# Performance work log

Measured on AMD Instinct MI355X. Metric: run time of the kernel, lower is better.

## Reference

```python
import jax, jax.numpy as jnp
import numpy as np


def _dsconv(x, dw_w, dw_b, pw_w, pw_b):
    # depthwise 3x3 (padding=1, stride=1) + pointwise 1x1, both with bias (PyTorch Conv2d default)
    C = x.shape[1]
    y = jax.lax.conv_general_dilated(
        x, dw_w, window_strides=(1, 1), padding=((1, 1), (1, 1)),
        dimension_numbers=('NCHW', 'OIHW', 'NCHW'), feature_group_count=C)
    y = y + dw_b[None, :, None, None]
    y = jnp.einsum('bchw,oc->bohw', y, pw_w) + pw_b[None, :, None, None]
    return y


def setup_inputs() -> dict:
    key = jax.random.key(0)
    ks = jax.random.split(key, 16)
    B, C, H, W = 8, 256, 64, 256
    inp = {"x": jax.random.normal(ks[0], (B, C, H, W), dtype=jnp.float32)}
    chans = [(C, 128), (128, 64), (64, 32), (32, 9)]
    ki = 1
    for li, (ci, co) in enumerate(chans, start=1):
        inp[f"dw{li}_w"] = jax.random.normal(ks[ki], (ci, 1, 3, 3), dtype=jnp.float32) / 3.0; ki += 1
        inp[f"dw{li}_b"] = jnp.zeros((ci,), dtype=jnp.float32)
        inp[f"pw{li}_w"] = jax.random.normal(ks[ki], (co, ci), dtype=jnp.float32) / jnp.sqrt(jnp.float32(ci)); ki += 1
        inp[f"pw{li}_b"] = jnp.zeros((co,), dtype=jnp.float32)
    return inp


def reference(x,
              dw1_w, dw1_b, pw1_w, pw1_b,
              dw2_w, dw2_b, pw2_w, pw2_b,
              dw3_w, dw3_b, pw3_w, pw3_b,
              dw4_w, dw4_b, pw4_w, pw4_b):
    # la_conv stack: DSConv->ReLU x3, final DSConv (no relu), out channels = 9
    a = jax.nn.relu(_dsconv(x, dw1_w, dw1_b, pw1_w, pw1_b))
    a = jax.nn.relu(_dsconv(a, dw2_w, dw2_b, pw2_w, pw2_b))
    a = jax.nn.relu(_dsconv(a, dw3_w, dw3_b, pw3_w, pw3_b))
    a = _dsconv(a, dw4_w, dw4_b, pw4_w, pw4_b)            # (B,9,H,W)
    attn = jax.nn.softmax(a, axis=1)                      # softmax over the 9 taps

    B, C, H, W = x.shape
    xpad = jnp.pad(x, ((0, 0), (0, 0), (1, 1), (1, 1)))
    # dynamic 3x3 conv: out[b,c,i,j] = sum_{ki,kj} xpad[b,c,i+ki,j+kj] * attn[b,ki*3+kj,i,j]
    out = jnp.zeros_like(x)
    for ki in range(3):
        for kj in range(3):
            out = out + xpad[:, :, ki:ki + H, kj:kj + W] * attn[:, ki * 3 + kj][:, None, :, :]

    char_attn = attn.transpose(0, 2, 3, 1).reshape(B, H, W, 3, 3)
    return out, char_attn
```

## Files before the change

kernel.cpp:

```cpp
#include <hip/hip_runtime.h>
#include <math.h>

#define BH_ 64
#define BW_ 256
constexpr size_t HW = (size_t)BH_ * BW_;

using f32x4   = __attribute__((ext_vector_type(4))) float;
using short8  = __attribute__((ext_vector_type(8))) short;
using short4v = __attribute__((ext_vector_type(4))) short;

__device__ __forceinline__ short f2bf(float f) {
    unsigned u = __float_as_uint(f);
    u += 0x7fffu + ((u >> 16) & 1u);
    return (short)(u >> 16);
}
__device__ __forceinline__ float bf2f(short s) {
    return __uint_as_float(((unsigned)(unsigned short)s) << 16);
}

__device__ __forceinline__ int xcd_swizzle() {
    const int rb  = blockIdx.x;
    const int cpx = gridDim.x >> 3;
    return (rb & 7) * cpx + (rb >> 3);
}

__global__ __launch_bounds__(256)
void prep_kernel(const float* __restrict__ p1,
                 const float* __restrict__ p2,
                 const float* __restrict__ p3,
                 short* __restrict__ wb1,
                 short* __restrict__ wb2,
                 float* __restrict__ wt3)
{
    int idx = blockIdx.x * 256 + threadIdx.x;
    if (idx < 128 * 256) {
        wb1[idx] = f2bf(p1[idx]);
    } else if (idx < 128 * 256 + 64 * 128) {
        int r = idx - 128 * 256;
        wb2[r] = f2bf(p2[r]);
    } else if (idx < 128 * 256 + 64 * 128 + 32 * 64) {
        int r = idx - (128 * 256 + 64 * 128);
        int ci = r / 32, co = r % 32;
        wt3[r] = p3[co * 64 + ci];
    }
}

template<int CI, int CO, bool INBF>
__global__ __launch_bounds__(256, 4)
void dsconv_mfma(const void* __restrict__ xin_,
                 const float* __restrict__ dww,
                 const float* __restrict__ dwb,
                 const short* __restrict__ wBf,
                 const float* __restrict__ pwb,
                 short* __restrict__ out)
{
    constexpr int CIC = 32;
    constexpr int PX  = 64;
    constexpr int NT  = CO / 16;
    constexpr int WNT = NT / 4;
    constexpr int ST  = CI + 8;
    constexpr int NC  = CI / CIC;
    static_assert(NT % 4 == 0 && CI % CIC == 0, "geometry");

    __shared__ short Abuf[PX * ST];

    const int t    = threadIdx.x;
    const int w    = t >> 6;
    const int lane = t & 63;
    const int bid  = xcd_swizzle();
    const int jt   = bid & 3;
    const int i    = (bid >> 2) & 63;
    const int b    = bid >> 8;
    const int j0   = jt * PX;

    const int ci_l = t >> 3;
    const int g    = t & 7;
    const int jq   = j0 + g * 8;
    const bool vtop = (i > 0), vbot = (i < BH_ - 1);

    const int lm = lane & 15;
    const int kb = lane >> 4;

    {
        const int aswz = ((jq >> 3) & 7) << 3;
        #pragma unroll
        for (int c = 0; c < NC; ++c) {
            const int cc = c * CIC;
            const int ci = cc + ci_l;

            float xw[3][10];
            #pragma unroll
            for (int di = 0; di < 3; ++di) {
                const bool ok = (di == 0) ? vtop : (di == 2) ? vbot : true;
                if (ok) {
                    if constexpr (INBF) {
                        const short* xp = (const short*)xin_ + ((size_t)b * CI + ci) * HW;
                        const short* xr = xp + (size_t)(i + di - 1) * BW_ + jq;
                        xw[di][0] = (jq > 0) ? bf2f(xr[-1]) : 0.f;
                        short8 S = *reinterpret_cast<const short8*>(xr);
                        #pragma unroll
                        for (int e = 0; e < 8; ++e) xw[di][1 + e] = bf2f(S[e]);
                        xw[di][9] = (jq + 8 < BW_) ? bf2f(xr[8]) : 0.f;
                    } else {
                        const float* xp = (const float*)xin_ + ((size_t)b * CI + ci) * HW;
                        const float* xr = xp + (size_t)(i + di - 1) * BW_ + jq;
                        xw[di][0] = (jq > 0) ? xr[-1] : 0.f;
                        float4 A = *reinterpret_cast<const float4*>(xr);
                        float4 Bq = *reinterpret_cast<const float4*>(xr + 4);
                        xw[di][1] = A.x; xw[di][2] = A.y; xw[di][3] = A.z; xw[di][4] = A.w;
                        xw[di][5] = Bq.x; xw[di][6] = Bq.y; xw[di][7] = Bq.z; xw[di][8] = Bq.w;
                        xw[di][9] = (jq + 8 < BW_) ? xr[8] : 0.f;
                    }
                } else {
                    #pragma unroll
                    for (int e = 0; e < 10; ++e) xw[di][e] = 0.f;
                }
            }

            const float* wkp = dww + ci * 9;
            float o[8];
            {
                const float dwbv = dwb[ci];
                #pragma unroll
                for (int e = 0; e < 8; ++e) o[e] = dwbv;
            }
            #pragma unroll
            for (int di = 0; di < 3; ++di) {
                const float w0 = wkp[di * 3 + 0];
                const float w1 = wkp[di * 3 + 1];
                const float w2 = wkp[di * 3 + 2];
                #pragma unroll
                for (int e = 0; e < 8; ++e)
                    o[e] += w0 * xw[di][e] + w1 * xw[di][e + 1] + w2 * xw[di][e + 2];
            }
            #pragma unroll
            for (int e = 0; e < 8; ++e) {
                int px = g * 8 + e;
                int sa = (px * ST + ci) ^ aswz;
                Abuf[sa] = f2bf(o[e]);
            }
        }
    }

    __syncthreads();

    f32x4 acc[4][WNT];
    #pragma unroll
    for (int q = 0; q < WNT; ++q) {
        float bv = pwb[(w * WNT + q) * 16 + lm];
        #pragma unroll
        for (int mt = 0; mt < 4; ++mt) {
            f32x4 z = {bv, bv, bv, bv};
            acc[mt][q] = z;
        }
    }

    const short* bbase[WNT];
    #pragma unroll
    for (int q = 0; q < WNT; ++q)
        bbase[q] = wBf + (size_t)((w * WNT + q) * 16 + lm) * CI + kb * 8;

    short8 bcur[WNT], bnxt[WNT];
    #pragma unroll
    for (int q = 0; q < WNT; ++q)
        bcur[q] = *reinterpret_cast<const short8*>(bbase[q]);

    #pragma unroll
    for (int c = 0; c < NC; ++c) {
        if (c + 1 < NC) {
            #pragma unroll
            for (int q = 0; q < WNT; ++q)
                bnxt[q] = *reinterpret_cast<const short8*>(bbase[q] + (c + 1) * CIC);
        }
        #pragma unroll
        for (int mt = 0; mt < 4; ++mt) {
            int px = mt * 16 + lm;
            int sa = (px * ST + c * CIC + kb * 8) ^ (((px >> 3) & 7) << 3);
            short8 af = *reinterpret_cast<const short8*>(&Abuf[sa]);
            #pragma unroll
            for (int q = 0; q < WNT; ++q)
                acc[mt][q] = __builtin_amdgcn_mfma_f32_16x16x32_bf16(
                    af, bcur[q], acc[mt][q], 0, 0, 0);
        }
        #pragma unroll
        for (int q = 0; q < WNT; ++q) bcur[q] = bnxt[q];
    }

    #pragma unroll
    for (int mt = 0; mt < 4; ++mt) {
        #pragma unroll
        for (int q = 0; q < WNT; ++q) {
            int co = (w * WNT + q) * 16 + lm;
            short* op = out + (((size_t)b * CO + co) * BH_ + i) * BW_
                        + j0 + mt * 16 + kb * 4;
            short4v v;
            v[0] = f2bf(fmaxf(acc[mt][q][0], 0.f));
            v[1] = f2bf(fmaxf(acc[mt][q][1], 0.f));
            v[2] = f2bf(fmaxf(acc[mt][q][2], 0.f));
            v[3] = f2bf(fmaxf(acc[mt][q][3], 0.f));
            *reinterpret_cast<short4v*>(op) = v;
        }
    }
}

template<int CI, int CO, int CPT>
__global__ __launch_bounds__(256, 4)
void dsconv_kernel(const short* __restrict__ xin,
                   const float* __restrict__ dww,
                   const float* __restrict__ dwb,
                   const float* __restrict__ wT,
                   const float* __restrict__ pwb,
                   short* __restrict__ out)
{
    constexpr int CIC = 32;
    constexpr int PX  = 64;
    static_assert(CO / CPT == 16, "co groups must be 16");

    __shared__ float dwbuf[CIC * PX];
    __shared__ float wbuf[CIC * CO];

    const int t   = threadIdx.x;
    const int bid = xcd_swizzle();
    const int jt  = bid & 3;
    const int i   = (bid >> 2) & 63;
    const int b   = bid >> 8;
    const int j0  = jt * PX;

    const int px_g = t & 15;
    const int co_g = t >> 4;
    const int co0  = co_g * CPT;
    const int p0   = px_g * 4;

    const int ci_local = t >> 3;
    const int g        = t & 7;
    const int jq       = j0 + g * 8;

    float acc[CPT][4];
    #pragma unroll
    for (int ii = 0; ii < CPT; ++ii) {
        float bv = pwb[co0 + ii];
        #pragma unroll
        for (int jj = 0; jj < 4; ++jj) acc[ii][jj] = bv;
    }

    for (int cc = 0; cc < CI; cc += CIC) {
        __syncthreads();
        {
            const float* src = wT + (size_t)cc * CO;
            #pragma unroll
            for (int idx = t * 4; idx < CIC * CO; idx += 1024)
                *reinterpret_cast<float4*>(&wbuf[idx]) =
                    *reinterpret_cast<const float4*>(&src[idx]);
        }
        {
            const int ci = cc + ci_local;
            const float* wk = dww + ci * 9;
            float w[9];
            #pragma unroll
            for (int k = 0; k < 9; ++k) w[k] = wk[k];
            float o[8];
            float bv = dwb[ci];
            #pragma unroll
            for (int e = 0; e < 8; ++e) o[e] = bv;

            const short* xp = xin + ((size_t)b * CI + ci) * HW;
            #pragma unroll
            for (int di = -1; di <= 1; ++di) {
                int ii2 = i + di;
                if ((unsigned)ii2 < (unsigned)BH_) {
                    const short* xr = xp + (size_t)ii2 * BW_ + jq;
                    float v[10];
                    v[0] = (jq > 0) ? bf2f(xr[-1]) : 0.f;
                    short8 S = *reinterpret_cast<const short8*>(xr);
                    #pragma unroll
                    for (int e = 0; e < 8; ++e) v[1 + e] = bf2f(S[e]);
                    v[9] = (jq + 8 < BW_) ? bf2f(xr[8]) : 0.f;
                    const float w0 = w[(di + 1) * 3 + 0];
                    const float w1 = w[(di + 1) * 3 + 1];
                    const float w2 = w[(di + 1) * 3 + 2];
                    #pragma unroll
                    for (int e = 0; e < 8; ++e)
                        o[e] += w0 * v[e] + w1 * v[e + 1] + w2 * v[e + 2];
                }
            }
            float4* dst = reinterpret_cast<float4*>(&dwbuf[ci_local * PX + g * 8]);
            dst[0] = make_float4(o[0], o[1], o[2], o[3]);
            dst[1] = make_float4(o[4], o[5], o[6], o[7]);
        }
        __syncthreads();

        #pragma unroll 4
        for (int k = 0; k < CIC; ++k) {
            float4 dq = *reinterpret_cast<const float4*>(&dwbuf[k * PX + p0]);
            float dv[4] = {dq.x, dq.y, dq.z, dq.w};
            float wv2[CPT];
            if constexpr (CPT == 2) {
                float2 wq = *reinterpret_cast<const float2*>(&wbuf[k * CO + co0]);
                wv2[0] = wq.x; wv2[1] = wq.y;
            } else {
                float4 wq = *reinterpret_cast<const float4*>(&wbuf[k * CO + co0]);
                #pragma unroll
                for (int ii = 0; ii < CPT && ii < 4; ++ii) wv2[ii] = (&wq.x)[ii];
            }
            #pragma unroll
            for (int ii = 0; ii < CPT; ++ii)
                #pragma unroll
                for (int jj = 0; jj < 4; ++jj)
                    acc[ii][jj] += wv2[ii] * dv[jj];
        }
    }

    #pragma unroll
    for (int ii = 0; ii < CPT; ++ii) {
        short4v v;
        v[0] = f2bf(fmaxf(acc[ii][0], 0.f));
        v[1] = f2bf(fmaxf(acc[ii][1], 0.f));
        v[2] = f2bf(fmaxf(acc[ii][2], 0.f));
        v[3] = f2bf(fmaxf(acc[ii][3], 0.f));
        short* op = out + (((size_t)b * CO + co0 + ii) * BH_ + i) * BW_ + j0 + p0;
        *reinterpret_cast<short4v*>(op) = v;
    }
}

__global__ __launch_bounds__(256, 4)
void final_kernel(const float* __restrict__ x,
                  const short* __restrict__ a3,
                  const float* __restrict__ dww,
                  const float* __restrict__ dwb,
                  const float* __restrict__ pww,
                  const float* __restrict__ pwb,
                  float* __restrict__ out,
                  float* __restrict__ chat)
{
    constexpr int PX = 64;
    __shared__ float dwbuf[32 * PX];
    __shared__ float attL[9][PX];

    const int t   = threadIdx.x;
    const int bid = xcd_swizzle();
    const int jt  = bid & 3;
    const int i   = (bid >> 2) & 63;
    const int b   = bid >> 8;
    const int j0  = jt * PX;
    const int g   = t & 7;
    const int jq  = j0 + g * 8;

    {
        const int ci = t >> 3;
        const float* wk = dww + ci * 9;
        float w[9];
        #pragma unroll
        for (int k = 0; k < 9; ++k) w[k] = wk[k];
        float o[8];
        float bv = dwb[ci];
        #pragma unroll
        for (int e = 0; e < 8; ++e) o[e] = bv;

        const short* xp = a3 + ((size_t)b * 32 + ci) * HW;
        #pragma unroll
        for (int di = -1; di <= 1; ++di) {
            int ii2 = i + di;
            if ((unsigned)ii2 < (unsigned)BH_) {
                const short* xr = xp + (size_t)ii2 * BW_ + jq;
                float v[10];
                v[0] = (jq > 0) ? bf2f(xr[-1]) : 0.f;
                short8 S = *reinterpret_cast<const short8*>(xr);
                #pragma unroll
                for (int e = 0; e < 8; ++e) v[1 + e] = bf2f(S[e]);
                v[9] = (jq + 8 < BW_) ? bf2f(xr[8]) : 0.f;
                const float w0 = w[(di + 1) * 3 + 0];
                const float w1 = w[(di + 1) * 3 + 1];
                const float w2 = w[(di + 1) * 3 + 2];
                #pragma unroll
                for (int e = 0; e < 8; ++e)
                    o[e] += w0 * v[e] + w1 * v[e + 1] + w2 * v[e + 2];
            }
        }
        float4* dst = reinterpret_cast<float4*>(&dwbuf[(t >> 3) * PX + g * 8]);
        dst[0] = make_float4(o[0], o[1], o[2], o[3]);
        dst[1] = make_float4(o[4], o[5], o[6], o[7]);
    }
    __syncthreads();

    for (int idx = t; idx < 9 * PX; idx += 256) {
        int co = idx >> 6;
        int px = idx & 63;
        float acc = pwb[co];
        #pragma unroll
        for (int ci = 0; ci < 32; ++ci)
            acc += pww[co * 32 + ci] * dwbuf[ci * PX + px];
        attL[co][px] = acc;
    }
    __syncthreads();

    if (t < PX) {
        float v[9];
        float m = -1e30f;
        #pragma unroll
        for (int k = 0; k < 9; ++k) { v[k] = attL[k][t]; m = fmaxf(m, v[k]); }
        float s = 0.f;
        #pragma unroll
        for (int k = 0; k < 9; ++k) { v[k] = __expf(v[k] - m); s += v[k]; }
        float inv = 1.f / s;
        #pragma unroll
        for (int k = 0; k < 9; ++k) attL[k][t] = v[k] * inv;
    }
    __syncthreads();

    {
        size_t base = (((size_t)b * BH_ + i) * BW_ + j0) * 9;
        for (int idx = t; idx < PX * 9; idx += 256)
            chat[base + idx] = attL[idx % 9][idx / 9];
    }

    float ar[9][8];
    #pragma unroll
    for (int k = 0; k < 9; ++k) {
        float4 a0 = *reinterpret_cast<const float4*>(&attL[k][g * 8]);
        float4 a1 = *reinterpret_cast<const float4*>(&attL[k][g * 8 + 4]);
        ar[k][0] = a0.x; ar[k][1] = a0.y; ar[k][2] = a0.z; ar[k][3] = a0.w;
        ar[k][4] = a1.x; ar[k][5] = a1.y; ar[k][6] = a1.z; ar[k][7] = a1.w;
    }

    const int c0 = t >> 3;
    for (int c = c0; c < 256; c += 32) {
        const float* xp = x + ((size_t)b * 256 + c) * HW;
        float v3[3][10];
        #pragma unroll
        for (int di = 0; di < 3; ++di) {
            int ii2 = i + di - 1;
            if ((unsigned)ii2 < (unsigned)BH_) {
                const float* xr = xp + (size_t)ii2 * BW_ + jq;
                v3[di][0] = (jq > 0) ? xr[-1] : 0.f;
                float4 A = *reinterpret_cast<const float4*>(xr);
                float4 Bq = *reinterpret_cast<const float4*>(xr + 4);
                v3[di][1] = A.x; v3[di][2] = A.y; v3[di][3] = A.z; v3[di][4] = A.w;
                v3[di][5] = Bq.x; v3[di][6] = Bq.y; v3[di][7] = Bq.z; v3[di][8] = Bq.w;
                v3[di][9] = (jq + 8 < BW_) ? xr[8] : 0.f;
            } else {
                #pragma unroll
                for (int e = 0; e < 10; ++e) v3[di][e] = 0.f;
            }
        }
        float o[8];
        #pragma unroll
        for (int e = 0; e < 8; ++e) o[e] = 0.f;
        #pragma unroll
        for (int di = 0; di < 3; ++di)
            #pragma unroll
            for (int dj = 0; dj < 3; ++dj)
                #pragma unroll
                for (int e = 0; e < 8; ++e)
                    o[e] += v3[di][e + dj] * ar[di * 3 + dj][e];
        float* op = out + ((size_t)b * 256 + c) * HW + (size_t)i * BW_ + jq;
        *reinterpret_cast<float4*>(op)     = make_float4(o[0], o[1], o[2], o[3]);
        *reinterpret_cast<float4*>(op + 4) = make_float4(o[4], o[5], o[6], o[7]);
    }
}

extern "C" void kernel_launch(void* const* d_in, const int* in_sizes, int n_in,
                              void* d_out, int out_size, void* d_ws, size_t ws_size,
                              hipStream_t stream)
{
    const float* x    = (const float*)d_in[0];
    const float* dw1w = (const float*)d_in[1];
    const float* dw1b = (const float*)d_in[2];
    const float* pw1w = (const float*)d_in[3];
    const float* pw1b = (const float*)d_in[4];
    const float* dw2w = (const float*)d_in[5];
    const float* dw2b = (const float*)d_in[6];
    const float* pw2w = (const float*)d_in[7];
    const float* pw2b = (const float*)d_in[8];
    const float* dw3w = (const float*)d_in[9];
    const float* dw3b = (const float*)d_in[10];
    const float* pw3w = (const float*)d_in[11];
    const float* pw3b = (const float*)d_in[12];
    const float* dw4w = (const float*)d_in[13];
    const float* dw4b = (const float*)d_in[14];
    const float* pw4w = (const float*)d_in[15];
    const float* pw4b = (const float*)d_in[16];

    float* outp = (float*)d_out;
    float* chat = outp + (size_t)8 * 256 * HW;

    short* wb1 = (short*)d_ws;
    short* wb2 = wb1 + 128 * 256;
    float* wt3 = (float*)((char*)d_ws + 81920);
    short* abase = (short*)((char*)d_ws + 90112);

    int kmax = 1;
    for (int k = 8; k >= 1; k >>= 1) {
        size_t need = 90112 + (size_t)k * (128 + 64) * HW * sizeof(short);
        if (need <= ws_size) { kmax = k; break; }
    }
    short* a1 = abase;
    short* a2 = a1 + (size_t)kmax * 128 * HW;
    short* a3 = a1;

    prep_kernel<<<(128 * 256 + 64 * 128 + 32 * 64 + 255) / 256, 256, 0, stream>>>(
        pw1w, pw2w, pw3w, wb1, wb2, wt3);

    for (int b0 = 0; b0 < 8; b0 += kmax) {
        int kc = (8 - b0 < kmax) ? (8 - b0) : kmax;
        const float* xb = x + (size_t)b0 * 256 * HW;
        int grid64 = kc * 256;

        dsconv_mfma<256, 128, false><<<grid64, 256, 0, stream>>>(
            xb, dw1w, dw1b, wb1, pw1b, a1);
        dsconv_mfma<128, 64, true><<<grid64, 256, 0, stream>>>(
            a1, dw2w, dw2b, wb2, pw2b, a2);
        dsconv_kernel<64, 32, 2><<<grid64, 256, 0, stream>>>(
            a2, dw3w, dw3b, wt3, pw3b, a3);
        final_kernel<<<grid64, 256, 0, stream>>>(
            xb, a3, dw4w, dw4b, pw4w, pw4b,
            outp + (size_t)b0 * 256 * HW, chat + (size_t)b0 * HW * 9);
    }
}
```

Before: 220.6 us.

## Fold depthwise weights into pointwise as nine-tap implicit GEMM on MFMA

The first two depthwise-separable convs are rewritten algebraically. The depthwise 3x3 filter is folded into the pointwise weights, giving nine per-tap bf16 matrices and a folded bias. Each block stages a 4-row halo tile of the bf16 input in LDS and runs nine MFMA passes, so the scalar depthwise FMA work is gone. Tiles now cover two output rows, which halves the grid and reuses the halo rows. The cost is nine times more MFMA work and weight traffic, input rounded to bf16 before the depthwise step, and a larger workspace; the final kernel's channel loop also gets unroll 2.

Result: slower. 493.6 us (+123.7%).

```diff
diff --git a/kernel.cpp b/kernel.cpp
--- a/kernel.cpp
+++ b/kernel.cpp
@@ -24,175 +24,181 @@
     return (rb & 7) * cpx + (rb >> 3);
 }
 
+constexpr int MK1_E = 9 * 128 * 256;
+constexpr int MK2_E = 9 * 64 * 128;
+
 __global__ __launch_bounds__(256)
-void prep_kernel(const float* __restrict__ p1,
-                 const float* __restrict__ p2,
-                 const float* __restrict__ p3,
-                 short* __restrict__ wb1,
-                 short* __restrict__ wb2,
+void prep_kernel(const float* __restrict__ pw1, const float* __restrict__ dw1w,
+                 const float* __restrict__ dw1b, const float* __restrict__ pw1b,
+                 const float* __restrict__ pw2, const float* __restrict__ dw2w,
+                 const float* __restrict__ dw2b, const float* __restrict__ pw2b,
+                 const float* __restrict__ pw3,
+                 short* __restrict__ mk1, short* __restrict__ mk2,
+                 float* __restrict__ b1, float* __restrict__ b2,
                  float* __restrict__ wt3)
 {
     int idx = blockIdx.x * 256 + threadIdx.x;
-    if (idx < 128 * 256) {
-        wb1[idx] = f2bf(p1[idx]);
-    } else if (idx < 128 * 256 + 64 * 128) {
-        int r = idx - 128 * 256;
-        wb2[r] = f2bf(p2[r]);
-    } else if (idx < 128 * 256 + 64 * 128 + 32 * 64) {
-        int r = idx - (128 * 256 + 64 * 128);
-        int ci = r / 32, co = r % 32;
-        wt3[r] = p3[co * 64 + ci];
+    if (idx < MK1_E) {
+        int k = idx >> 15;
+        int r = idx & 32767;
+        int co = r >> 8, ci = r & 255;
+        mk1[idx] = f2bf(pw1[co * 256 + ci] * dw1w[ci * 9 + k]);
+    } else if (idx < MK1_E + MK2_E) {
+        int r2 = idx - MK1_E;
+        int k = r2 >> 13;
+        int rr = r2 & 8191;
+        int co = rr >> 7, ci = rr & 127;
+        mk2[r2] = f2bf(pw2[co * 128 + ci] * dw2w[ci * 9 + k]);
+    } else if (idx < MK1_E + MK2_E + 128) {
+        int co = idx - (MK1_E + MK2_E);
+        float s = pw1b[co];
+        for (int ci = 0; ci < 256; ++ci) s += pw1[co * 256 + ci] * dw1b[ci];
+        b1[co] = s;
+    } else if (idx < MK1_E + MK2_E + 192) {
+        int co = idx - (MK1_E + MK2_E + 128);
+        float s = pw2b[co];
+        for (int ci = 0; ci < 128; ++ci) s += pw2[co * 128 + ci] * dw2b[ci];
+        b2[co] = s;
+    } else if (idx < MK1_E + MK2_E + 192 + 2048) {
+        int r = idx - (MK1_E + MK2_E + 192);
+        int ci = r >> 5, co = r & 31;
+        wt3[r] = pw3[co * 64 + ci];
     }
 }
 
 template<int CI, int CO, bool INBF>
 __global__ __launch_bounds__(256, 4)
-void dsconv_mfma(const void* __restrict__ xin_,
-                 const float* __restrict__ dww,
-                 const float* __restrict__ dwb,
-                 const short* __restrict__ wBf,
-                 const float* __restrict__ pwb,
-                 short* __restrict__ out)
+void dsconv_mfma9(const void* __restrict__ xin_,
+                  const short* __restrict__ Mk,
+                  const float* __restrict__ biasE,
+                  short* __restrict__ out)
 {
     constexpr int CIC = 32;
-    constexpr int PX  = 64;
     constexpr int NT  = CO / 16;
     constexpr int WNT = NT / 4;
-    constexpr int ST  = CI + 8;
-    constexpr int NC  = CI / CIC;
-    static_assert(NT % 4 == 0 && CI % CIC == 0, "geometry");
-
-    __shared__ short Abuf[PX * ST];
+    constexpr int MT  = 8;
+    constexpr size_t TAPS = (size_t)CO * CI;
+    static_assert(CI % CIC == 0 && NT % 4 == 0, "geometry");
+
+    __shared__ short Ax[4 * 66 * 64];
 
     const int t    = threadIdx.x;
     const int w    = t >> 6;
     const int lane = t & 63;
     const int bid  = xcd_swizzle();
     const int jt   = bid & 3;
-    const int i    = (bid >> 2) & 63;
-    const int b    = bid >> 8;
-    const int j0   = jt * PX;
+    const int it   = (bid >> 2) & 31;
+    const int b    = bid >> 7;
+    const int j0   = jt * 64;
+    const int i0   = it * 2;
 
     const int ci_l = t >> 3;
     const int g    = t & 7;
     const int jq   = j0 + g * 8;
-    const bool vtop = (i > 0), vbot = (i < BH_ - 1);
 
     const int lm = lane & 15;
     const int kb = lane >> 4;
 
-    {
-        const int aswz = ((jq >> 3) & 7) << 3;
-        #pragma unroll
-        for (int c = 0; c < NC; ++c) {
-            const int cc = c * CIC;
+    auto AADDR = [](int r, int P, int s8) -> int {
+        int X = (((P >> 3) ^ P) & 7) << 3;
+        return (r * 66 + P) * 64 + (s8 ^ X);
+    };
+
+    f32x4 acc[MT][WNT];
+    #pragma unroll
+    for (int q = 0; q < WNT; ++q) {
+        float bv = biasE[(w * WNT + q) * 16 + lm];
+        #pragma unroll
+        for (int mt = 0; mt < MT; ++mt) {
+            f32x4 z = {bv, bv, bv, bv};
+            acc[mt][q] = z;
+        }
+    }
+
+    const short* mkq[WNT];
+    #pragma unroll
+    for (int q = 0; q < WNT; ++q)
+        mkq[q] = Mk + (size_t)((w * WNT + q) * 16 + lm) * CI + kb * 8;
+
+    for (int cc = 0; cc < CI; cc += CIC) {
+        __syncthreads();
+
+        {
             const int ci = cc + ci_l;
-
-            float xw[3][10];
-            #pragma unroll
-            for (int di = 0; di < 3; ++di) {
-                const bool ok = (di == 0) ? vtop : (di == 2) ? vbot : true;
-                if (ok) {
+            #pragma unroll
+            for (int r = 0; r < 4; ++r) {
+                const int ig = i0 + r - 1;
+                short sv[10];
+                if ((unsigned)ig < (unsigned)BH_) {
                     if constexpr (INBF) {
-                        const short* xp = (const short*)xin_ + ((size_t)b * CI + ci) * HW;
-                        const short* xr = xp + (size_t)(i + di - 1) * BW_ + jq;
-                        xw[di][0] = (jq > 0) ? bf2f(xr[-1]) : 0.f;
+                        const short* xr = (const short*)xin_
+                            + ((size_t)b * CI + ci) * HW + (size_t)ig * BW_ + jq;
+                        sv[0] = (jq > 0) ? xr[-1] : (short)0;
                         short8 S = *reinterpret_cast<const short8*>(xr);
                         #pragma unroll
-                        for (int e = 0; e < 8; ++e) xw[di][1 + e] = bf2f(S[e]);
-                        xw[di][9] = (jq + 8 < BW_) ? bf2f(xr[8]) : 0.f;
+                        for (int e = 0; e < 8; ++e) sv[1 + e] = S[e];
+                        sv[9] = (jq + 8 < BW_) ? xr[8] : (short)0;
                     } else {
-                        const float* xp = (const float*)xin_ + ((size_t)b * CI + ci) * HW;
-                        const float* xr = xp + (size_t)(i + di - 1) * BW_ + jq;
-                        xw[di][0] = (jq > 0) ? xr[-1] : 0.f;
+                        const float* xr = (const float*)xin_
+                            + ((size_t)b * CI + ci) * HW + (size_t)ig * BW_ + jq;
+                        sv[0] = f2bf((jq > 0) ? xr[-1] : 0.f);
                         float4 A = *reinterpret_cast<const float4*>(xr);
                         float4 Bq = *reinterpret_cast<const float4*>(xr + 4);
-                        xw[di][1] = A.x; xw[di][2] = A.y; xw[di][3] = A.z; xw[di][4] = A.w;
-                        xw[di][5] = Bq.x; xw[di][6] = Bq.y; xw[di][7] = Bq.z; xw[di][8] = Bq.w;
-                        xw[di][9] = (jq + 8 < BW_) ? xr[8] : 0.f;
+                        sv[1] = f2bf(A.x); sv[2] = f2bf(A.y);
+                        sv[3] = f2bf(A.z); sv[4] = f2bf(A.w);
+                        sv[5] = f2bf(Bq.x); sv[6] = f2bf(Bq.y);
+                        sv[7] = f2bf(Bq.z); sv[8] = f2bf(Bq.w);
+                        sv[9] = f2bf((jq + 8 < BW_) ? xr[8] : 0.f);
                     }
                 } else {
                     #pragma unroll
-                    for (int e = 0; e < 10; ++e) xw[di][e] = 0.f;
+                    for (int k = 0; k < 10; ++k) sv[k] = 0;
                 }
-            }
-
-            const float* wkp = dww + ci * 9;
-            float o[8];
-            {
-                const float dwbv = dwb[ci];
-                #pragma unroll
-                for (int e = 0; e < 8; ++e) o[e] = dwbv;
-            }
-            #pragma unroll
-            for (int di = 0; di < 3; ++di) {
-                const float w0 = wkp[di * 3 + 0];
-                const float w1 = wkp[di * 3 + 1];
-                const float w2 = wkp[di * 3 + 2];
                 #pragma unroll
                 for (int e = 0; e < 8; ++e)
-                    o[e] += w0 * xw[di][e] + w1 * xw[di][e + 1] + w2 * xw[di][e + 2];
-            }
-            #pragma unroll
-            for (int e = 0; e < 8; ++e) {
-                int px = g * 8 + e;
-                int sa = (px * ST + ci) ^ aswz;
-                Abuf[sa] = f2bf(o[e]);
-            }
-        }
-    }
-
-    __syncthreads();
-
-    f32x4 acc[4][WNT];
+                    Ax[AADDR(r, g * 8 + e + 1, ci_l)] = sv[e + 1];
+                if (g == 0) Ax[AADDR(r, 0,  ci_l)] = sv[0];
+                if (g == 7) Ax[AADDR(r, 65, ci_l)] = sv[9];
+            }
+        }
+        __syncthreads();
+
+        short8 bf[WNT], bfn[WNT];
+        #pragma unroll
+        for (int q = 0; q < WNT; ++q)
+            bf[q] = *reinterpret_cast<const short8*>(mkq[q] + cc);
+        #pragma unroll
+        for (int tap = 0; tap < 9; ++tap) {
+            if (tap < 8) {
+                #pragma unroll
+                for (int q = 0; q < WNT; ++q)
+                    bfn[q] = *reinterpret_cast<const short8*>(
+                        mkq[q] + (size_t)(tap + 1) * TAPS + cc);
+            }
+            const int di = tap / 3, dj = tap % 3;
+            #pragma unroll
+            for (int mt = 0; mt < MT; ++mt) {
+                const int rl = mt >> 2;
+                short8 af = *reinterpret_cast<const short8*>(
+                    &Ax[AADDR(rl + di, (mt & 3) * 16 + lm + dj, kb * 8)]);
+                #pragma unroll
+                for (int q = 0; q < WNT; ++q)
+                    acc[mt][q] = __builtin_amdgcn_mfma_f32_16x16x32_bf16(
+                        af, bf[q], acc[mt][q], 0, 0, 0);
+            }
+            #pragma unroll
+            for (int q = 0; q < WNT; ++q) bf[q] = bfn[q];
+        }
+    }
+
     #pragma unroll
-    for (int q = 0; q < WNT; ++q) {
-        float bv = pwb[(w * WNT + q) * 16 + lm];
-        #pragma unroll
-        for (int mt = 0; mt < 4; ++mt) {
-            f32x4 z = {bv, bv, bv, bv};
-            acc[mt][q] = z;
-        }
-    }
-
-    const short* bbase[WNT];
-    #pragma unroll
-    for (int q = 0; q < WNT; ++q)
-        bbase[q] = wBf + (size_t)((w * WNT + q) * 16 + lm) * CI + kb * 8;
-
-    short8 bcur[WNT], bnxt[WNT];
-    #pragma unroll
-    for (int q = 0; q < WNT; ++q)
-        bcur[q] = *reinterpret_cast<const short8*>(bbase[q]);
-
-    #pragma unroll
-    for (int c = 0; c < NC; ++c) {
-        if (c + 1 < NC) {
-            #pragma unroll
-            for (int q = 0; q < WNT; ++q)
-                bnxt[q] = *reinterpret_cast<const short8*>(bbase[q] + (c + 1) * CIC);
-        }
-        #pragma unroll
-        for (int mt = 0; mt < 4; ++mt) {
-            int px = mt * 16 + lm;
-            int sa = (px * ST + c * CIC + kb * 8) ^ (((px >> 3) & 7) << 3);
-            short8 af = *reinterpret_cast<const short8*>(&Abuf[sa]);
-            #pragma unroll
-            for (int q = 0; q < WNT; ++q)
-                acc[mt][q] = __builtin_amdgcn_mfma_f32_16x16x32_bf16(
-                    af, bcur[q], acc[mt][q], 0, 0, 0);
-        }
-        #pragma unroll
-        for (int q = 0; q < WNT; ++q) bcur[q] = bnxt[q];
-    }
-
-    #pragma unroll
-    for (int mt = 0; mt < 4; ++mt) {
+    for (int mt = 0; mt < MT; ++mt) {
+        const int rl = mt >> 2;
+        const int jl = (mt & 3) * 16 + kb * 4;
         #pragma unroll
         for (int q = 0; q < WNT; ++q) {
             int co = (w * WNT + q) * 16 + lm;
-            short* op = out + (((size_t)b * CO + co) * BH_ + i) * BW_
-                        + j0 + mt * 16 + kb * 4;
+            short* op = out + (((size_t)b * CO + co) * BH_ + i0 + rl) * BW_ + j0 + jl;
             short4v v;
             v[0] = f2bf(fmaxf(acc[mt][q][0], 0.f));
             v[1] = f2bf(fmaxf(acc[mt][q][1], 0.f));
@@ -423,6 +429,7 @@
     }
 
     const int c0 = t >> 3;
+    #pragma unroll 2
     for (int c = c0; c < 256; c += 32) {
         const float* xp = x + ((size_t)b * 256 + c) * HW;
         float v3[3][10];
@@ -483,32 +490,36 @@
     float* outp = (float*)d_out;
     float* chat = outp + (size_t)8 * 256 * HW;
 
-    short* wb1 = (short*)d_ws;
-    short* wb2 = wb1 + 128 * 256;
-    float* wt3 = (float*)((char*)d_ws + 81920);
-    short* abase = (short*)((char*)d_ws + 90112);
+    short* mk1 = (short*)d_ws;
+    short* mk2 = (short*)((char*)d_ws + 589824);
+    float* b1  = (float*)((char*)d_ws + 737280);
+    float* b2  = (float*)((char*)d_ws + 737792);
+    float* wt3 = (float*)((char*)d_ws + 738048);
+    short* abase = (short*)((char*)d_ws + 746496);
 
     int kmax = 1;
     for (int k = 8; k >= 1; k >>= 1) {
-        size_t need = 90112 + (size_t)k * (128 + 64) * HW * sizeof(short);
+        size_t need = 746496 + (size_t)k * (128 + 64) * HW * sizeof(short);
         if (need <= ws_size) { kmax = k; break; }
     }
     short* a1 = abase;
     short* a2 = a1 + (size_t)kmax * 128 * HW;
     short* a3 = a1;
 
-    prep_kernel<<<(128 * 256 + 64 * 128 + 32 * 64 + 255) / 256, 256, 0, stream>>>(
-        pw1w, pw2w, pw3w, wb1, wb2, wt3);
+    prep_kernel<<<(MK1_E + MK2_E + 192 + 2048 + 255) / 256, 256, 0, stream>>>(
+        pw1w, dw1w, dw1b, pw1b, pw2w, dw2w, dw2b, pw2b, pw3w,
+        mk1, mk2, b1, b2, wt3);
 
     for (int b0 = 0; b0 < 8; b0 += kmax) {
         int kc = (8 - b0 < kmax) ? (8 - b0) : kmax;
         const float* xb = x + (size_t)b0 * 256 * HW;
-        int grid64 = kc * 256;
-
-        dsconv_mfma<256, 128, false><<<grid64, 256, 0, stream>>>(
-            xb, dw1w, dw1b, wb1, pw1b, a1);
-        dsconv_mfma<128, 64, true><<<grid64, 256, 0, stream>>>(
-            a1, dw2w, dw2b, wb2, pw2b, a2);
+        int grid128 = kc * 128;
+        int grid64  = kc * 256;
+
+        dsconv_mfma9<256, 128, false><<<grid128, 256, 0, stream>>>(
+            xb, mk1, b1, a1);
+        dsconv_mfma9<128, 64, true><<<grid128, 256, 0, stream>>>(
+            a1, mk2, b2, a2);
         dsconv_kernel<64, 32, 2><<<grid64, 256, 0, stream>>>(
             a2, dw3w, dw3b, wt3, pw3b, a3);
         final_kernel<<<grid64, 256, 0, stream>>>(
```
